# Kernel optimization log

Hardware: AMD Instinct MI355X
Metric: run time of the kernel (lower is better)

## Reference

```python
import jax, jax.numpy as jnp
import numpy as np

N = 50000          # nodes
E = 800000         # edges (avg degree 16)
IN = 128           # input feature dim
HID = 64           # hidden dim per head
HEADS = 2          # attention heads (all but last layer)
OUT = 64           # out_dim (last layer, 1 head)
NC = 2             # num_classes
NEG_SLOPE = 0.2    # dgl GATConv leaky_relu slope


def setup_inputs() -> dict:
    key = jax.random.key(0)
    ks = jax.random.split(key, 20)
    rn = lambda k, shape, s=0.05: (jax.random.normal(k, shape, jnp.float32) * s)
    W_IO = HID * HEADS  # 128, width between GAT layers
    return {
        "x": rn(ks[0], (N, IN), 1.0),
        "src": jax.random.randint(ks[1], (E,), 0, N, dtype=jnp.int32),
        "dst": jax.random.randint(ks[2], (E,), 0, N, dtype=jnp.int32),
        # embedding_h: Linear(IN, HID*HEADS)
        "W_emb": rn(ks[3], (IN, W_IO)),
        "b_emb": jnp.zeros((W_IO,), jnp.float32),
        # GAT layer 0: in 128 -> 2 heads x 64
        "W0": rn(ks[4], (W_IO, HEADS * HID)),
        "al0": rn(ks[5], (HEADS, HID)),
        "ar0": rn(ks[6], (HEADS, HID)),
        "b0": jnp.zeros((HEADS * HID,), jnp.float32),
        # GAT layer 1: in 128 -> 2 heads x 64
        "W1": rn(ks[7], (W_IO, HEADS * HID)),
        "al1": rn(ks[8], (HEADS, HID)),
        "ar1": rn(ks[9], (HEADS, HID)),
        "b1": jnp.zeros((HEADS * HID,), jnp.float32),
        # GAT layer 2 (last): in 128 -> 1 head x OUT
        "W2": rn(ks[10], (W_IO, 1 * OUT)),
        "al2": rn(ks[11], (1, OUT)),
        "ar2": rn(ks[12], (1, OUT)),
        "b2": jnp.zeros((OUT,), jnp.float32),
        # edge scorer: Linear(2*OUT, NC)
        "Ws": rn(ks[13], (2 * OUT, NC)),
        "bs": jnp.zeros((NC,), jnp.float32),
    }


def gat_layer(h, src, dst, W, al, ar, b):
    """dgl GATConv + elu (GATLayer with batch_norm=False, residual=False)."""
    heads, out = al.shape
    feat = (h @ W).reshape(-1, heads, out)            # [N,H,D]
    el = jnp.sum(feat * al, axis=-1)                  # [N,H]
    er = jnp.sum(feat * ar, axis=-1)                  # [N,H]
    e = jax.nn.leaky_relu(el[src] + er[dst], NEG_SLOPE)  # [E,H]
    # edge softmax over incoming edges of each dst node
    emax = jax.ops.segment_max(e, dst, num_segments=N)   # [N,H]
    ex = jnp.exp(e - emax[dst])                          # [E,H]
    denom = jax.ops.segment_sum(ex, dst, num_segments=N) # [N,H]
    alpha = ex / jnp.where(denom[dst] > 0, denom[dst], 1.0)
    msg = feat[src] * alpha[:, :, None]                  # [E,H,D]
    rst = jax.ops.segment_sum(msg, dst, num_segments=N)  # [N,H,D]
    rst = rst.reshape(-1, heads * out) + b
    return jax.nn.elu(rst)


def reference(x, W_emb, b_emb, W0, al0, ar0, b0, W1, al1, ar1, b1,
              W2, al2, ar2, b2, Ws, bs, src, dst):
    h = x @ W_emb + b_emb                    # embedding_h (dropout p -> eval/identity)
    h = gat_layer(h, src, dst, W0, al0, ar0, b0)
    h = gat_layer(h, src, dst, W1, al1, ar1, b1)
    h = gat_layer(h, src, dst, W2, al2, ar2, b2)   # [N, OUT]
    # edge scorer on the scored subgraph: concat(src_h, dst_h) -> Linear
    he = jnp.concatenate([h[src], h[dst]], axis=1)  # [E, 2*OUT]
    return he @ Ws + bs                             # [E, NC]
```

## Files before the change

### kernel.cpp

```cpp
#include <hip/hip_runtime.h>
#include <hip/hip_bf16.h>
#include <math.h>


constexpr float SLOPE = 0.2f;

__device__ __forceinline__ float b2f(unsigned short u) {
  union { unsigned int i; float f; } v;
  v.i = ((unsigned int)u) << 16;
  return v.f;
}
__device__ __forceinline__ unsigned short f2b(float f) {
  unsigned int x = __float_as_uint(f);
  unsigned int r = (x + 0x7fffu + ((x >> 16) & 1u)) >> 16;
  return (unsigned short)r;
}

template<int M, bool OUTBF16>
__global__ __launch_bounds__(512)
void gemm_k128(const float* __restrict__ X, const float* __restrict__ W,
               const float* __restrict__ bias,
               const float* __restrict__ al, const float* __restrict__ ar,
               void* __restrict__ Yv, float* __restrict__ el,
               float* __restrict__ er, int N) {
  constexpr int K = 128;
  constexpr int BM = 64;
  constexpr int CPT = M / 32;
  constexpr int H = M / 64;
  constexpr int WH4 = (64 * M) / 4;
  __shared__ __align__(16) float Xs[BM][K];
  __shared__ __align__(16) float Wsm[64][M];

  const int tid = threadIdx.x;
  const int row0 = blockIdx.x * BM;

  #pragma unroll
  for (int j = 0; j < (BM * K) / (512 * 4); ++j) {
    int lin = tid + j * 512;
    int r = lin >> 5;
    int c4 = lin & 31;
    int gr = row0 + r;
    float4 v = make_float4(0.f, 0.f, 0.f, 0.f);
    if (gr < N) v = reinterpret_cast<const float4*>(X + (size_t)gr * K)[c4];
    reinterpret_cast<float4*>(&Xs[r][0])[c4] = v;
  }
  #pragma unroll
  for (int j = 0; j < WH4 / 512; ++j) {
    int lin = tid + j * 512;
    reinterpret_cast<float4*>(&Wsm[0][0])[lin] =
        reinterpret_cast<const float4*>(W)[lin];
  }
  __syncthreads();

  const int tr = tid >> 5;
  const int tc = tid & 31;

  float acc[4][CPT];
  #pragma unroll
  for (int i = 0; i < 4; ++i)
    #pragma unroll
    for (int c = 0; c < CPT; ++c) acc[i][c] = 0.f;

  #pragma unroll
  for (int half = 0; half < 2; ++half) {
    #pragma unroll 2
    for (int k4l = 0; k4l < 16; ++k4l) {
      const int kg = half * 64 + k4l * 4;
      float4 xv[4];
      #pragma unroll
      for (int i = 0; i < 4; ++i)
        xv[i] = *reinterpret_cast<const float4*>(&Xs[tr * 4 + i][kg]);
      if constexpr (CPT == 4) {
        float4 wv[4];
        #pragma unroll
        for (int kk = 0; kk < 4; ++kk)
          wv[kk] = *reinterpret_cast<const float4*>(&Wsm[k4l * 4 + kk][tc * 4]);
        #pragma unroll
        for (int i = 0; i < 4; ++i) {
          const float* xp = reinterpret_cast<const float*>(&xv[i]);
          #pragma unroll
          for (int kk = 0; kk < 4; ++kk) {
            acc[i][0] += xp[kk] * wv[kk].x;
            acc[i][1] += xp[kk] * wv[kk].y;
            acc[i][2] += xp[kk] * wv[kk].z;
            acc[i][3] += xp[kk] * wv[kk].w;
          }
        }
      } else {
        float2 wv[4];
        #pragma unroll
        for (int kk = 0; kk < 4; ++kk)
          wv[kk] = *reinterpret_cast<const float2*>(&Wsm[k4l * 4 + kk][tc * 2]);
        #pragma unroll
        for (int i = 0; i < 4; ++i) {
          const float* xp = reinterpret_cast<const float*>(&xv[i]);
          #pragma unroll
          for (int kk = 0; kk < 4; ++kk) {
            acc[i][0] += xp[kk] * wv[kk].x;
            acc[i][1] += xp[kk] * wv[kk].y;
          }
        }
      }
    }
    if (half == 0) {
      __syncthreads();
      #pragma unroll
      for (int j = 0; j < WH4 / 512; ++j) {
        int lin = tid + j * 512;
        reinterpret_cast<float4*>(&Wsm[0][0])[lin] =
            reinterpret_cast<const float4*>(W)[WH4 + lin];
      }
      __syncthreads();
    }
  }

  float bv[CPT];
  #pragma unroll
  for (int c = 0; c < CPT; ++c) bv[c] = bias ? bias[tc * CPT + c] : 0.f;

  #pragma unroll
  for (int i = 0; i < 4; ++i) {
    int gr = row0 + tr * 4 + i;
    if (gr < N) {
      if constexpr (OUTBF16) {
        unsigned short* Yb = reinterpret_cast<unsigned short*>(Yv);
        if constexpr (CPT == 4) {
          ushort4 o;
          o.x = f2b(acc[i][0] + bv[0]);
          o.y = f2b(acc[i][1] + bv[1]);
          o.z = f2b(acc[i][2] + bv[2]);
          o.w = f2b(acc[i][3] + bv[3]);
          *reinterpret_cast<ushort4*>(&Yb[(size_t)gr * M + tc * 4]) = o;
        } else {
          ushort2 o;
          o.x = f2b(acc[i][0] + bv[0]);
          o.y = f2b(acc[i][1] + bv[1]);
          *reinterpret_cast<ushort2*>(&Yb[(size_t)gr * M + tc * 2]) = o;
        }
      } else {
        float* Y = reinterpret_cast<float*>(Yv);
        if constexpr (CPT == 4) {
          float4 o = make_float4(acc[i][0] + bv[0], acc[i][1] + bv[1],
                                 acc[i][2] + bv[2], acc[i][3] + bv[3]);
          *reinterpret_cast<float4*>(&Y[(size_t)gr * M + tc * 4]) = o;
        } else {
          float2 o = make_float2(acc[i][0] + bv[0], acc[i][1] + bv[1]);
          *reinterpret_cast<float2*>(&Y[(size_t)gr * M + tc * 2]) = o;
        }
      }
    }
  }

  if (al != nullptr) {
    int head, colbase;
    if constexpr (CPT == 4) { head = tc >> 4; colbase = tc * 4 - head * 64; }
    else                    { head = 0;       colbase = tc * 2; }
    float av[CPT], rv[CPT];
    #pragma unroll
    for (int c = 0; c < CPT; ++c) {
      av[c] = al[head * 64 + colbase + c];
      rv[c] = ar[head * 64 + colbase + c];
    }
    #pragma unroll
    for (int i = 0; i < 4; ++i) {
      float pl = 0.f, pr = 0.f;
      #pragma unroll
      for (int c = 0; c < CPT; ++c) {
        pl += acc[i][c] * av[c];
        pr += acc[i][c] * rv[c];
      }
      if constexpr (CPT == 4) {
        #pragma unroll
        for (int off = 1; off < 16; off <<= 1) {
          pl += __shfl_xor(pl, off);
          pr += __shfl_xor(pr, off);
        }
        if ((tc & 15) == 0) {
          int gr = row0 + tr * 4 + i;
          if (gr < N) { el[gr * H + head] = pl; er[gr * H + head] = pr; }
        }
      } else {
        #pragma unroll
        for (int off = 1; off < 32; off <<= 1) {
          pl += __shfl_xor(pl, off);
          pr += __shfl_xor(pr, off);
        }
        if (tc == 0) {
          int gr = row0 + tr * 4 + i;
          if (gr < N) { el[gr] = pl; er[gr] = pr; }
        }
      }
    }
  }
}

__global__ void count_dst(const int* __restrict__ dst, int* __restrict__ cnt,
                          int E) {
  int i = blockIdx.x * blockDim.x + threadIdx.x;
  if (i < E) atomicAdd(&cnt[dst[i]], 1);
}

__global__ void scan1(const int* __restrict__ cnt, int* __restrict__ outv,
                      int* __restrict__ bsum, int n) {
  __shared__ int sm[256];
  int tid = threadIdx.x;
  int base = blockIdx.x * 1024 + tid * 4;
  int pre[4];
  int s = 0;
  #pragma unroll
  for (int j = 0; j < 4; ++j) {
    int idx = base + j;
    int v = (idx < n) ? cnt[idx] : 0;
    pre[j] = s;
    s += v;
  }
  sm[tid] = s;
  __syncthreads();
  for (int off = 1; off < 256; off <<= 1) {
    int a = (tid >= off) ? sm[tid - off] : 0;
    __syncthreads();
    sm[tid] += a;
    __syncthreads();
  }
  int excl = sm[tid] - s;
  #pragma unroll
  for (int j = 0; j < 4; ++j) {
    int idx = base + j;
    if (idx < n) outv[idx] = excl + pre[j];
  }
  if (tid == 255) bsum[blockIdx.x] = sm[255];
}

__global__ void scan2(const int* __restrict__ bsum, int* __restrict__ btop,
                      int nb, int* __restrict__ row_last) {
  if (threadIdx.x == 0 && blockIdx.x == 0) {
    int s = 0;
    for (int i = 0; i < nb; ++i) { btop[i] = s; s += bsum[i]; }
    *row_last = s;
  }
}

__global__ void scan3(int* __restrict__ rp, int* __restrict__ cur,
                      const int* __restrict__ btop, int n) {
  int i = blockIdx.x * blockDim.x + threadIdx.x;
  if (i < n) {
    int v = rp[i] + btop[i >> 10];
    rp[i] = v;
    cur[i] = v;
  }
}

__global__ __launch_bounds__(256)
void scatter_edges(const int* __restrict__ src, const int* __restrict__ dst,
                   int* __restrict__ cur, int* __restrict__ s_csr, int E) {
  int cls = blockIdx.x & 7;
  int grp = blockIdx.x >> 3;
  int nGrp = gridDim.x >> 3;
  for (int base = grp * 256; base < E; base += nGrp * 256) {
    int i = base + threadIdx.x;
    if (i < E) {
      int d = dst[i];
      if (((d >> 4) & 7) == cls) {
        int p = atomicAdd(&cur[d], 1);
        s_csr[p] = src[i];
      }
    }
  }
}

template<int H>
__global__ __launch_bounds__(256)
void edge_prep(const int* __restrict__ s_csr, const float* __restrict__ el,
               const float* __restrict__ er, const int* __restrict__ rp,
               float2* __restrict__ edat, int N, int E) {
  int tid = threadIdx.x;
  int node = blockIdx.x * 16 + (tid >> 4);
  int sl = tid & 15;
  if (node >= N) return;
  int beg = rp[node];
  int end = rp[node + 1];
  if constexpr (H == 2) {
    float2 re = reinterpret_cast<const float2*>(er)[node];
    for (int p = beg + sl; p < end; p += 16) {
      int s = s_csr[p];
      float2 le = reinterpret_cast<const float2*>(el)[s];
      float e0 = le.x + re.x;
      float e1 = le.y + re.y;
      e0 = e0 > 0.f ? e0 : SLOPE * e0;
      e1 = e1 > 0.f ? e1 : SLOPE * e1;
      float sb = __int_as_float(s);
      edat[p] = make_float2(__expf(e0), sb);
      edat[(size_t)E + p] = make_float2(__expf(e1), sb);
    }
  } else {
    float re = er[node];
    for (int p = beg + sl; p < end; p += 16) {
      int s = s_csr[p];
      float ev = el[s] + re;
      ev = ev > 0.f ? ev : SLOPE * ev;
      edat[p] = make_float2(__expf(ev), __int_as_float(s));
    }
  }
}

template<int H, bool SCORE>
__global__ __launch_bounds__(256)
void gat_aggregate(const unsigned short* __restrict__ featb,
                   const float2* __restrict__ edat,
                   const float* __restrict__ bias,
                   const int* __restrict__ row_ptr,
                   float* __restrict__ hout,
                   const float* __restrict__ Wsc,
                   float* __restrict__ ps, float* __restrict__ pd,
                   int N, int E) {
  int tid = threadIdx.x;
  int pid = blockIdx.x * 16 + (tid >> 4);
  int sl = tid & 15;
  const int NH = N * H;
  bool live = pid < NH;
  int pc = live ? pid : 0;
  int node, head;
  if constexpr (H == 2) { node = pc >> 1; head = pc & 1; }
  else                  { node = pc;      head = 0; }
  int beg = live ? row_ptr[node] : 0;
  int end = live ? row_ptr[node + 1] : 0;

  const int rowoff = head * 64 + sl * 4;
  const float2* edath = edat + (size_t)head * E;

  float4 acc = make_float4(0.f, 0.f, 0.f, 0.f);
  float den = 0.f;

  for (int p = beg; p < end; p += 8) {
    #pragma unroll
    for (int j = 0; j < 8; ++j) {
      int q = p + j;
      int qc = q < end ? q : end - 1;
      float2 ed = edath[qc];
      float ex = q < end ? ed.x : 0.f;
      int s = __float_as_int(ed.y);
      ushort4 u = *reinterpret_cast<const ushort4*>(
          &featb[(size_t)s * (H * 64) + rowoff]);
      den += ex;
      acc.x += ex * b2f(u.x);
      acc.y += ex * b2f(u.y);
      acc.z += ex * b2f(u.z);
      acc.w += ex * b2f(u.w);
    }
  }

  if (live) {
    float inv = 1.f / (den > 0.f ? den : 1.f);
    float4 bv = reinterpret_cast<const float4*>(bias)[head * 16 + sl];
    float4 r;
    r.x = acc.x * inv + bv.x;
    r.y = acc.y * inv + bv.y;
    r.z = acc.z * inv + bv.z;
    r.w = acc.w * inv + bv.w;
    r.x = r.x > 0.f ? r.x : expm1f(r.x);
    r.y = r.y > 0.f ? r.y : expm1f(r.y);
    r.z = r.z > 0.f ? r.z : expm1f(r.z);
    r.w = r.w > 0.f ? r.w : expm1f(r.w);

    if constexpr (!SCORE) {
      reinterpret_cast<float4*>(hout)[(size_t)pid * 16 + sl] = r;
    } else {
      float s0 = r.x * Wsc[(4 * sl + 0) * 2] + r.y * Wsc[(4 * sl + 1) * 2] +
                 r.z * Wsc[(4 * sl + 2) * 2] + r.w * Wsc[(4 * sl + 3) * 2];
      float s1 = r.x * Wsc[(4 * sl + 0) * 2 + 1] + r.y * Wsc[(4 * sl + 1) * 2 + 1] +
                 r.z * Wsc[(4 * sl + 2) * 2 + 1] + r.w * Wsc[(4 * sl + 3) * 2 + 1];
      float d0 = r.x * Wsc[(64 + 4 * sl + 0) * 2] + r.y * Wsc[(64 + 4 * sl + 1) * 2] +
                 r.z * Wsc[(64 + 4 * sl + 2) * 2] + r.w * Wsc[(64 + 4 * sl + 3) * 2];
      float d1 = r.x * Wsc[(64 + 4 * sl + 0) * 2 + 1] + r.y * Wsc[(64 + 4 * sl + 1) * 2 + 1] +
                 r.z * Wsc[(64 + 4 * sl + 2) * 2 + 1] + r.w * Wsc[(64 + 4 * sl + 3) * 2 + 1];
      #pragma unroll
      for (int off = 1; off < 16; off <<= 1) {
        s0 += __shfl_xor(s0, off);
        s1 += __shfl_xor(s1, off);
        d0 += __shfl_xor(d0, off);
        d1 += __shfl_xor(d1, off);
      }
      if (sl == 0) {
        ps[node * 2 + 0] = s0;
        ps[node * 2 + 1] = s1;
        pd[node * 2 + 0] = d0;
        pd[node * 2 + 1] = d1;
      }
    }
  }
}

__global__ void score_out(const int* __restrict__ src,
                          const int* __restrict__ dst,
                          const float* __restrict__ ps,
                          const float* __restrict__ pd,
                          const float* __restrict__ bs,
                          float* __restrict__ out, int E) {
  int i = blockIdx.x * blockDim.x + threadIdx.x;
  if (i < E) {
    int s = src[i], d = dst[i];
    float2 a = *reinterpret_cast<const float2*>(ps + (size_t)s * 2);
    float2 b = *reinterpret_cast<const float2*>(pd + (size_t)d * 2);
    float2 o;
    o.x = a.x + b.x + bs[0];
    o.y = a.y + b.y + bs[1];
    *reinterpret_cast<float2*>(out + (size_t)i * 2) = o;
  }
}

extern "C" void kernel_launch(void* const* d_in, const int* in_sizes, int n_in,
                              void* d_out, int out_size, void* d_ws,
                              size_t ws_size, hipStream_t stream) {
  const float* x    = (const float*)d_in[0];
  const int*   src  = (const int*)d_in[1];
  const int*   dst  = (const int*)d_in[2];
  const float* Wemb = (const float*)d_in[3];
  const float* bemb = (const float*)d_in[4];
  const float* W0   = (const float*)d_in[5];
  const float* al0  = (const float*)d_in[6];
  const float* ar0  = (const float*)d_in[7];
  const float* b0   = (const float*)d_in[8];
  const float* W1   = (const float*)d_in[9];
  const float* al1  = (const float*)d_in[10];
  const float* ar1  = (const float*)d_in[11];
  const float* b1   = (const float*)d_in[12];
  const float* W2   = (const float*)d_in[13];
  const float* al2  = (const float*)d_in[14];
  const float* ar2  = (const float*)d_in[15];
  const float* b2   = (const float*)d_in[16];
  const float* Wsc  = (const float*)d_in[17];
  const float* bsc  = (const float*)d_in[18];

  const int N = in_sizes[0] / 128;
  const int E = in_sizes[1];
  float* out = (float*)d_out;

  char* w = (char*)d_ws;
  float*  A    = (float*)w;  w += (size_t)N * 128 * 4;
  float2* edat = (float2*)w; w += (size_t)E * 2 * 8;
  unsigned short* Bb = (unsigned short*)w; w += (size_t)N * 128 * 2;
  float* el  = (float*)w; w += (size_t)N * 2 * 4;
  float* er  = (float*)w; w += (size_t)N * 2 * 4;
  float* ps  = (float*)w; w += (size_t)N * 2 * 4;
  float* pd  = (float*)w; w += (size_t)N * 2 * 4;
  int* s_csr = (int*)w;   w += (size_t)E * 4;
  int* cnt   = (int*)w;   w += (size_t)N * 4;
  int* rp    = (int*)w;   w += (size_t)(N + 4) * 4;
  int* cur   = (int*)w;   w += (size_t)N * 4;
  int* bsum  = (int*)w;   w += 4096;
  int* btop  = (int*)w;   w += 4096;

  hipMemsetAsync(cnt, 0, (size_t)N * 4, stream);
  count_dst<<<(E + 255) / 256, 256, 0, stream>>>(dst, cnt, E);
  int nb = (N + 1023) / 1024;
  scan1<<<nb, 256, 0, stream>>>(cnt, rp, bsum, N);
  scan2<<<1, 64, 0, stream>>>(bsum, btop, nb, rp + N);
  scan3<<<(N + 255) / 256, 256, 0, stream>>>(rp, cur, btop, N);
  scatter_edges<<<2048, 256, 0, stream>>>(src, dst, cur, s_csr, E);

  const int gb = (N + 63) / 64;
  const int nbk = (N + 15) / 16;
  const int pb2 = (N * 2 + 15) / 16;
  const int pb1 = (N * 1 + 15) / 16;

  gemm_k128<128, false><<<gb, 512, 0, stream>>>(x, Wemb, bemb, nullptr, nullptr,
                                                A, nullptr, nullptr, N);

  gemm_k128<128, true><<<gb, 512, 0, stream>>>(A, W0, nullptr, al0, ar0,
                                               Bb, el, er, N);
  edge_prep<2><<<nbk, 256, 0, stream>>>(s_csr, el, er, rp, edat, N, E);
  gat_aggregate<2, false><<<pb2, 256, 0, stream>>>(Bb, edat, b0, rp, A,
                                                   nullptr, nullptr, nullptr,
                                                   N, E);
  gemm_k128<128, true><<<gb, 512, 0, stream>>>(A, W1, nullptr, al1, ar1,
                                               Bb, el, er, N);
  edge_prep<2><<<nbk, 256, 0, stream>>>(s_csr, el, er, rp, edat, N, E);
  gat_aggregate<2, false><<<pb2, 256, 0, stream>>>(Bb, edat, b1, rp, A,
                                                   nullptr, nullptr, nullptr,
                                                   N, E);
  gemm_k128<64, true><<<gb, 512, 0, stream>>>(A, W2, nullptr, al2, ar2,
                                              Bb, el, er, N);
  edge_prep<1><<<nbk, 256, 0, stream>>>(s_csr, el, er, rp, edat, N, E);
  gat_aggregate<1, true><<<pb1, 256, 0, stream>>>(Bb, edat, b2, rp, nullptr,
                                                  Wsc, ps, pd, N, E);

  score_out<<<(E + 255) / 256, 256, 0, stream>>>(src, dst, ps, pd, bsc, out, E);
}
```

Baseline: 440.6 us.

## Replace FP32 SIMT GEMMs with bf16 MFMA kernels and store activations in bf16

The four dense N×128 GEMMs now run on MFMA 16x16x32 bf16 instructions. Weights are pre-transposed and converted to bf16 by a small prep kernel, and A operands are read straight from global memory with no LDS staging. The inter-layer activation buffer becomes bf16, so the aggregation kernels write half the bytes and the next GEMM reads half. This costs extra rounding of the input, the weights and the hidden activations, and adds four tiny prep launches per call.

```diff
diff --git a/kernel.cpp b/kernel.cpp
--- a/kernel.cpp
+++ b/kernel.cpp
@@ -4,6 +4,9 @@
 
 
 constexpr float SLOPE = 0.2f;
+
+typedef __attribute__((ext_vector_type(8))) short bf16x8;
+typedef __attribute__((ext_vector_type(4))) float f32x4;
 
 __device__ __forceinline__ float b2f(unsigned short u) {
   union { unsigned int i; float f; } v;
@@ -16,178 +19,115 @@
   return (unsigned short)r;
 }
 
-template<int M, bool OUTBF16>
-__global__ __launch_bounds__(512)
-void gemm_k128(const float* __restrict__ X, const float* __restrict__ W,
+__global__ void prep_wt(const float* __restrict__ W,
+                        unsigned short* __restrict__ Wt, int M) {
+  int i = blockIdx.x * 256 + threadIdx.x;
+  if (i < 128 * M) {
+    int k = i / M, m = i - k * M;
+    Wt[m * 128 + k] = f2b(W[i]);
+  }
+}
+
+template<int M, bool AF32>
+__global__ __launch_bounds__(256)
+void gemm_mfma(const void* __restrict__ Xv,
+               const unsigned short* __restrict__ Wt,
                const float* __restrict__ bias,
                const float* __restrict__ al, const float* __restrict__ ar,
-               void* __restrict__ Yv, float* __restrict__ el,
-               float* __restrict__ er, int N) {
-  constexpr int K = 128;
-  constexpr int BM = 64;
-  constexpr int CPT = M / 32;
+               unsigned short* __restrict__ Yb,
+               float* __restrict__ el, float* __restrict__ er, int N) {
+  constexpr int NT = M / 16;
   constexpr int H = M / 64;
-  constexpr int WH4 = (64 * M) / 4;
-  __shared__ __align__(16) float Xs[BM][K];
-  __shared__ __align__(16) float Wsm[64][M];
 
   const int tid = threadIdx.x;
-  const int row0 = blockIdx.x * BM;
-
-  #pragma unroll
-  for (int j = 0; j < (BM * K) / (512 * 4); ++j) {
-    int lin = tid + j * 512;
-    int r = lin >> 5;
-    int c4 = lin & 31;
-    int gr = row0 + r;
-    float4 v = make_float4(0.f, 0.f, 0.f, 0.f);
-    if (gr < N) v = reinterpret_cast<const float4*>(X + (size_t)gr * K)[c4];
-    reinterpret_cast<float4*>(&Xs[r][0])[c4] = v;
-  }
-  #pragma unroll
-  for (int j = 0; j < WH4 / 512; ++j) {
-    int lin = tid + j * 512;
-    reinterpret_cast<float4*>(&Wsm[0][0])[lin] =
-        reinterpret_cast<const float4*>(W)[lin];
-  }
-  __syncthreads();
-
-  const int tr = tid >> 5;
-  const int tc = tid & 31;
-
-  float acc[4][CPT];
-  #pragma unroll
-  for (int i = 0; i < 4; ++i)
+  const int wave = tid >> 6;
+  const int lane = tid & 63;
+  const int r = lane & 15;
+  const int kg = lane >> 4;
+  const int rowbase = blockIdx.x * 64 + wave * 16;
+  int grow = rowbase + r;
+  int growc = grow < N ? grow : N - 1;
+
+  f32x4 acc[NT];
+  #pragma unroll
+  for (int t = 0; t < NT; ++t) acc[t] = (f32x4){0.f, 0.f, 0.f, 0.f};
+
+  #pragma unroll
+  for (int kk = 0; kk < 4; ++kk) {
+    const int k0 = kk * 32 + kg * 8;
+    bf16x8 a;
+    if constexpr (AF32) {
+      const float* X = (const float*)Xv;
+      const float4* xp =
+          reinterpret_cast<const float4*>(X + (size_t)growc * 128 + k0);
+      float4 x0 = xp[0], x1 = xp[1];
+      a[0] = (short)f2b(x0.x); a[1] = (short)f2b(x0.y);
+      a[2] = (short)f2b(x0.z); a[3] = (short)f2b(x0.w);
+      a[4] = (short)f2b(x1.x); a[5] = (short)f2b(x1.y);
+      a[6] = (short)f2b(x1.z); a[7] = (short)f2b(x1.w);
+    } else {
+      const unsigned short* Xb = (const unsigned short*)Xv;
+      a = *reinterpret_cast<const bf16x8*>(Xb + (size_t)growc * 128 + k0);
+    }
     #pragma unroll
-    for (int c = 0; c < CPT; ++c) acc[i][c] = 0.f;
-
-  #pragma unroll
-  for (int half = 0; half < 2; ++half) {
-    #pragma unroll 2
-    for (int k4l = 0; k4l < 16; ++k4l) {
-      const int kg = half * 64 + k4l * 4;
-      float4 xv[4];
+    for (int t = 0; t < NT; ++t) {
+      bf16x8 b = *reinterpret_cast<const bf16x8*>(
+          Wt + (size_t)(t * 16 + r) * 128 + k0);
+      acc[t] = __builtin_amdgcn_mfma_f32_16x16x32_bf16(a, b, acc[t], 0, 0, 0);
+    }
+  }
+
+  float bv[NT];
+  #pragma unroll
+  for (int t = 0; t < NT; ++t) bv[t] = bias ? bias[t * 16 + r] : 0.f;
+  float alv[NT], arv[NT];
+  if (al != nullptr) {
+    #pragma unroll
+    for (int t = 0; t < NT; ++t) {
+      alv[t] = al[t * 16 + r];
+      arv[t] = ar[t * 16 + r];
+    }
+  }
+
+  #pragma unroll
+  for (int j = 0; j < 4; ++j) {
+    int orow = rowbase + kg * 4 + j;
+    bool ok = orow < N;
+    if (ok) {
       #pragma unroll
-      for (int i = 0; i < 4; ++i)
-        xv[i] = *reinterpret_cast<const float4*>(&Xs[tr * 4 + i][kg]);
-      if constexpr (CPT == 4) {
-        float4 wv[4];
+      for (int t = 0; t < NT; ++t)
+        Yb[(size_t)orow * M + t * 16 + r] = f2b(acc[t][j] + bv[t]);
+    }
+    if (al != nullptr) {
+      float pl0 = 0.f, pr0 = 0.f, pl1 = 0.f, pr1 = 0.f;
+      #pragma unroll
+      for (int t = 0; t < 4; ++t) {
+        pl0 += acc[t][j] * alv[t];
+        pr0 += acc[t][j] * arv[t];
+      }
+      if constexpr (H == 2) {
         #pragma unroll
-        for (int kk = 0; kk < 4; ++kk)
-          wv[kk] = *reinterpret_cast<const float4*>(&Wsm[k4l * 4 + kk][tc * 4]);
-        #pragma unroll
-        for (int i = 0; i < 4; ++i) {
-          const float* xp = reinterpret_cast<const float*>(&xv[i]);
-          #pragma unroll
-          for (int kk = 0; kk < 4; ++kk) {
-            acc[i][0] += xp[kk] * wv[kk].x;
-            acc[i][1] += xp[kk] * wv[kk].y;
-            acc[i][2] += xp[kk] * wv[kk].z;
-            acc[i][3] += xp[kk] * wv[kk].w;
-          }
+        for (int t = 4; t < 8; ++t) {
+          pl1 += acc[t][j] * alv[t];
+          pr1 += acc[t][j] * arv[t];
         }
-      } else {
-        float2 wv[4];
-        #pragma unroll
-        for (int kk = 0; kk < 4; ++kk)
-          wv[kk] = *reinterpret_cast<const float2*>(&Wsm[k4l * 4 + kk][tc * 2]);
-        #pragma unroll
-        for (int i = 0; i < 4; ++i) {
-          const float* xp = reinterpret_cast<const float*>(&xv[i]);
-          #pragma unroll
-          for (int kk = 0; kk < 4; ++kk) {
-            acc[i][0] += xp[kk] * wv[kk].x;
-            acc[i][1] += xp[kk] * wv[kk].y;
-          }
+      }
+      #pragma unroll
+      for (int off = 1; off < 16; off <<= 1) {
+        pl0 += __shfl_xor(pl0, off);
+        pr0 += __shfl_xor(pr0, off);
+        if constexpr (H == 2) {
+          pl1 += __shfl_xor(pl1, off);
+          pr1 += __shfl_xor(pr1, off);
         }
       }
-    }
-    if (half == 0) {
-      __syncthreads();
-      #pragma unroll
-      for (int j = 0; j < WH4 / 512; ++j) {
-        int lin = tid + j * 512;
-        reinterpret_cast<float4*>(&Wsm[0][0])[lin] =
-            reinterpret_cast<const float4*>(W)[WH4 + lin];
-      }
-      __syncthreads();
-    }
-  }
-
-  float bv[CPT];
-  #pragma unroll
-  for (int c = 0; c < CPT; ++c) bv[c] = bias ? bias[tc * CPT + c] : 0.f;
-
-  #pragma unroll
-  for (int i = 0; i < 4; ++i) {
-    int gr = row0 + tr * 4 + i;
-    if (gr < N) {
-      if constexpr (OUTBF16) {
-        unsigned short* Yb = reinterpret_cast<unsigned short*>(Yv);
-        if constexpr (CPT == 4) {
-          ushort4 o;
-          o.x = f2b(acc[i][0] + bv[0]);
-          o.y = f2b(acc[i][1] + bv[1]);
-          o.z = f2b(acc[i][2] + bv[2]);
-          o.w = f2b(acc[i][3] + bv[3]);
-          *reinterpret_cast<ushort4*>(&Yb[(size_t)gr * M + tc * 4]) = o;
+      if (r == 0 && ok) {
+        if constexpr (H == 2) {
+          el[orow * 2 + 0] = pl0; el[orow * 2 + 1] = pl1;
+          er[orow * 2 + 0] = pr0; er[orow * 2 + 1] = pr1;
         } else {
-          ushort2 o;
-          o.x = f2b(acc[i][0] + bv[0]);
-          o.y = f2b(acc[i][1] + bv[1]);
-          *reinterpret_cast<ushort2*>(&Yb[(size_t)gr * M + tc * 2]) = o;
-        }
-      } else {
-        float* Y = reinterpret_cast<float*>(Yv);
-        if constexpr (CPT == 4) {
-          float4 o = make_float4(acc[i][0] + bv[0], acc[i][1] + bv[1],
-                                 acc[i][2] + bv[2], acc[i][3] + bv[3]);
-          *reinterpret_cast<float4*>(&Y[(size_t)gr * M + tc * 4]) = o;
-        } else {
-          float2 o = make_float2(acc[i][0] + bv[0], acc[i][1] + bv[1]);
-          *reinterpret_cast<float2*>(&Y[(size_t)gr * M + tc * 2]) = o;
-        }
-      }
-    }
-  }
-
-  if (al != nullptr) {
-    int head, colbase;
-    if constexpr (CPT == 4) { head = tc >> 4; colbase = tc * 4 - head * 64; }
-    else                    { head = 0;       colbase = tc * 2; }
-    float av[CPT], rv[CPT];
-    #pragma unroll
-    for (int c = 0; c < CPT; ++c) {
-      av[c] = al[head * 64 + colbase + c];
-      rv[c] = ar[head * 64 + colbase + c];
-    }
-    #pragma unroll
-    for (int i = 0; i < 4; ++i) {
-      float pl = 0.f, pr = 0.f;
-      #pragma unroll
-      for (int c = 0; c < CPT; ++c) {
-        pl += acc[i][c] * av[c];
-        pr += acc[i][c] * rv[c];
-      }
-      if constexpr (CPT == 4) {
-        #pragma unroll
-        for (int off = 1; off < 16; off <<= 1) {
-          pl += __shfl_xor(pl, off);
-          pr += __shfl_xor(pr, off);
-        }
-        if ((tc & 15) == 0) {
-          int gr = row0 + tr * 4 + i;
-          if (gr < N) { el[gr * H + head] = pl; er[gr * H + head] = pr; }
-        }
-      } else {
-        #pragma unroll
-        for (int off = 1; off < 32; off <<= 1) {
-          pl += __shfl_xor(pl, off);
-          pr += __shfl_xor(pr, off);
-        }
-        if (tc == 0) {
-          int gr = row0 + tr * 4 + i;
-          if (gr < N) { el[gr] = pl; er[gr] = pr; }
+          el[orow] = pl0;
+          er[orow] = pr0;
         }
       }
     }
@@ -309,7 +249,7 @@
                    const float2* __restrict__ edat,
                    const float* __restrict__ bias,
                    const int* __restrict__ row_ptr,
-                   float* __restrict__ hout,
+                   unsigned short* __restrict__ houtb,
                    const float* __restrict__ Wsc,
                    float* __restrict__ ps, float* __restrict__ pd,
                    int N, int E) {
@@ -363,7 +303,9 @@
     r.w = r.w > 0.f ? r.w : expm1f(r.w);
 
     if constexpr (!SCORE) {
-      reinterpret_cast<float4*>(hout)[(size_t)pid * 16 + sl] = r;
+      ushort4 o;
+      o.x = f2b(r.x); o.y = f2b(r.y); o.z = f2b(r.z); o.w = f2b(r.w);
+      *reinterpret_cast<ushort4*>(&houtb[(size_t)pid * 64 + sl * 4]) = o;
     } else {
       float s0 = r.x * Wsc[(4 * sl + 0) * 2] + r.y * Wsc[(4 * sl + 1) * 2] +
                  r.z * Wsc[(4 * sl + 2) * 2] + r.w * Wsc[(4 * sl + 3) * 2];
@@ -436,9 +378,13 @@
   float* out = (float*)d_out;
 
   char* w = (char*)d_ws;
-  float*  A    = (float*)w;  w += (size_t)N * 128 * 4;
   float2* edat = (float2*)w; w += (size_t)E * 2 * 8;
+  unsigned short* Ab = (unsigned short*)w; w += (size_t)N * 128 * 2;
   unsigned short* Bb = (unsigned short*)w; w += (size_t)N * 128 * 2;
+  unsigned short* WembT = (unsigned short*)w; w += 128 * 128 * 2;
+  unsigned short* W0T   = (unsigned short*)w; w += 128 * 128 * 2;
+  unsigned short* W1T   = (unsigned short*)w; w += 128 * 128 * 2;
+  unsigned short* W2T   = (unsigned short*)w; w += 128 * 64 * 2;
   float* el  = (float*)w; w += (size_t)N * 2 * 4;
   float* er  = (float*)w; w += (size_t)N * 2 * 4;
   float* ps  = (float*)w; w += (size_t)N * 2 * 4;
@@ -450,6 +396,11 @@
   int* bsum  = (int*)w;   w += 4096;
   int* btop  = (int*)w;   w += 4096;
 
+  prep_wt<<<(128 * 128 + 255) / 256, 256, 0, stream>>>(Wemb, WembT, 128);
+  prep_wt<<<(128 * 128 + 255) / 256, 256, 0, stream>>>(W0, W0T, 128);
+  prep_wt<<<(128 * 128 + 255) / 256, 256, 0, stream>>>(W1, W1T, 128);
+  prep_wt<<<(128 * 64 + 255) / 256, 256, 0, stream>>>(W2, W2T, 64);
+
   hipMemsetAsync(cnt, 0, (size_t)N * 4, stream);
   count_dst<<<(E + 255) / 256, 256, 0, stream>>>(dst, cnt, E);
   int nb = (N + 1023) / 1024;
@@ -463,23 +414,24 @@
   const int pb2 = (N * 2 + 15) / 16;
   const int pb1 = (N * 1 + 15) / 16;
 
-  gemm_k128<128, false><<<gb, 512, 0, stream>>>(x, Wemb, bemb, nullptr, nullptr,
-                                                A, nullptr, nullptr, N);
-
-  gemm_k128<128, true><<<gb, 512, 0, stream>>>(A, W0, nullptr, al0, ar0,
-                                               Bb, el, er, N);
+  gemm_mfma<128, true><<<gb, 256, 0, stream>>>(x, WembT, bemb, nullptr,
+                                               nullptr, Ab, nullptr, nullptr,
+                                               N);
+
+  gemm_mfma<128, false><<<gb, 256, 0, stream>>>(Ab, W0T, nullptr, al0, ar0,
+                                                Bb, el, er, N);
   edge_prep<2><<<nbk, 256, 0, stream>>>(s_csr, el, er, rp, edat, N, E);
-  gat_aggregate<2, false><<<pb2, 256, 0, stream>>>(Bb, edat, b0, rp, A,
+  gat_aggregate<2, false><<<pb2, 256, 0, stream>>>(Bb, edat, b0, rp, Ab,
                                                    nullptr, nullptr, nullptr,
                                                    N, E);
-  gemm_k128<128, true><<<gb, 512, 0, stream>>>(A, W1, nullptr, al1, ar1,
-                                               Bb, el, er, N);
+  gemm_mfma<128, false><<<gb, 256, 0, stream>>>(Ab, W1T, nullptr, al1, ar1,
+                                                Bb, el, er, N);
   edge_prep<2><<<nbk, 256, 0, stream>>>(s_csr, el, er, rp, edat, N, E);
-  gat_aggregate<2, false><<<pb2, 256, 0, stream>>>(Bb, edat, b1, rp, A,
+  gat_aggregate<2, false><<<pb2, 256, 0, stream>>>(Bb, edat, b1, rp, Ab,
                                                    nullptr, nullptr, nullptr,
                                                    N, E);
-  gemm_k128<64, true><<<gb, 512, 0, stream>>>(A, W2, nullptr, al2, ar2,
-                                              Bb, el, er, N);
+  gemm_mfma<64, false><<<gb, 256, 0, stream>>>(Ab, W2T, nullptr, al2, ar2,
+                                               Bb, el, er, N);
   edge_prep<1><<<nbk, 256, 0, stream>>>(s_csr, el, er, rp, edat, N, E);
   gat_aggregate<1, true><<<pb1, 256, 0, stream>>>(Bb, edat, b2, rp, nullptr,
                                                   Wsc, ps, pd, N, E);
```

New measurement: 414.1 us. 6.0% less time.
